# Kernel tuning notes

Hardware: AMD Instinct MI355X
Metric: run time of the kernel (lower is better)

The kernel has to match this reference:

```python
import jax, jax.numpy as jnp
import numpy as np

EMBED, VOCAB, NUM_DIGEST, EXPAND = 128, 50257, 4, 4


def _mueller_hash(k):
    # https://stackoverflow.com/a/12996028 , uint32 wraparound semantics
    k = (k >> np.uint32(16) ^ k) * np.uint32(73244475)
    k = (k >> np.uint32(16) ^ k) * np.uint32(73244475)
    k = k >> np.uint32(16) ^ k
    return k


def setup_inputs() -> dict:
    key = jax.random.key(0)
    k_tok, k_tab, k_w1, k_w2 = jax.random.split(key, 4)
    # bloom ledger hash indices (exact replication of bloom_ledger)
    ids = np.arange(VOCAB, dtype=np.uint32)
    i_list, j_list = [], []
    for _ in range(NUM_DIGEST):
        ids = _mueller_hash(ids)
        i_list.append(ids % VOCAB)
        ids = _mueller_hash(ids)
        j_list.append(ids % VOCAB)
    bloom_i = jnp.asarray(np.concatenate(i_list).astype(np.int32))
    bloom_j = jnp.asarray(np.concatenate(j_list).astype(np.int32))
    hidden = EMBED * EXPAND
    return {
        "tokens": jax.random.randint(k_tok, (8, 4096), 0, VOCAB, dtype=jnp.int32),
        "table": jax.random.normal(k_tab, (VOCAB, EMBED), jnp.float32) / np.sqrt(EMBED),
        "bloom_i": bloom_i,
        "bloom_j": bloom_j,
        "w1": jax.random.normal(k_w1, (EMBED, hidden), jnp.float32) / np.sqrt(EMBED),
        "b1": jnp.zeros((hidden,), jnp.float32),
        "w2": jax.random.normal(k_w2, (hidden, EMBED), jnp.float32) / np.sqrt(hidden),
        "b2": jnp.zeros((EMBED,), jnp.float32),
    }


def reference(tokens, table, bloom_i, bloom_j, w1, b1, w2, b2):
    vocab = table.shape[0]
    num_digest = bloom_i.shape[0] // vocab
    scale = jnp.asarray(1.0 / np.sqrt(num_digest), table.dtype)
    # bloom @ table as a scatter-add: A[i] += scale * table[j]  -> [vocab, embed]
    agg = jnp.zeros_like(table).at[bloom_i].add(scale * table[bloom_j])
    # one_hot(tokens) @ (bloom @ table) == row gather
    x = agg[tokens]                      # [B, S, embed]
    h = jax.nn.gelu(x @ w1 + b1)         # [B, S, hidden]
    return h @ w2 + b2                   # [B, S, embed]
```

## Files before the change

kernel.cpp:

```cpp
#include <hip/hip_runtime.h>
#include <hip/hip_bf16.h>
#include <stdint.h>

#define EMBED  128
#define HIDDEN 512
#define TB     64
#define HHALF  256
#define CAP    32

typedef __attribute__((ext_vector_type(8))) short short8v;
typedef __attribute__((ext_vector_type(4))) float f32x4;

__device__ __forceinline__ ushort f2bf(float f) {
    uint32_t b = __float_as_uint(f);
    uint32_t r = (b + 0x7FFFu + ((b >> 16) & 1u)) >> 16;
    return (ushort)r;
}

__device__ __forceinline__ float gelu_fast(float x) {
    float x2 = x * x;
    float u  = x * fmaf(0.035677408136f, x2, 0.7978845608f);
    float t  = __expf(2.0f * u);
    return x - x * __frcp_rn(t + 1.0f);
}

__global__ __launch_bounds__(256)
void prep_kernel(const float* __restrict__ w1, const float* __restrict__ w2,
                 ushort* __restrict__ W1t, ushort* __restrict__ W2t,
                 int* __restrict__ cnt, int vocab) {
    __shared__ float T[32][33];
    int b = blockIdx.x;
    int t = threadIdx.x;
    if (b < 128) {
        const float* in; ushort* outp; int inCols, outCols, tr, tc;
        if (b < 64) {
            in = w1; outp = W1t; inCols = 512; outCols = 128;
            tr = b >> 4; tc = b & 15;
        } else {
            int b2 = b - 64;
            in = w2; outp = W2t; inCols = 128; outCols = 512;
            tr = b2 >> 2; tc = b2 & 3;
        }
        int r  = t >> 3;
        int c4 = (t & 7) * 4;
        float4 v = *(const float4*)&in[(size_t)(tr * 32 + r) * inCols + tc * 32 + c4];
        T[c4 + 0][r] = v.x; T[c4 + 1][r] = v.y; T[c4 + 2][r] = v.z; T[c4 + 3][r] = v.w;
        __syncthreads();
        ushort o[4];
        #pragma unroll
        for (int i = 0; i < 4; ++i) o[i] = f2bf(T[r][c4 + i]);
        *(ushort4*)&outp[(size_t)(tc * 32 + r) * outCols + tr * 32 + c4] = *(ushort4*)o;
    } else {
        int i = (b - 128) * 256 + t;
        if (i < vocab) cnt[i] = 0;
    }
}

__global__ __launch_bounds__(256)
void bucket_kernel(const int* __restrict__ bi, const int* __restrict__ bj,
                   int* __restrict__ cnt, int* __restrict__ csr, int nk) {
    int k = blockIdx.x * blockDim.x + threadIdx.x;
    if (k >= nk) return;
    int i = bi[k];
    int slot = atomicAdd(&cnt[i], 1);
    if (slot < CAP) csr[(size_t)i * CAP + slot] = bj[k];
}

__global__ __launch_bounds__(512)
void mlp_mfma_kernel(const int*    __restrict__ tokens,
                     const float*  __restrict__ table,
                     const int*    __restrict__ cnt,
                     const int*    __restrict__ csr,
                     const ushort* __restrict__ W1t,
                     const ushort* __restrict__ W2t,
                     const float*  __restrict__ b1,
                     const float*  __restrict__ b2,
                     float*        __restrict__ out) {
    __shared__ ushort Xs[TB * EMBED];
    __shared__ ushort Hs[TB * HHALF];

    const int t    = threadIdx.x;
    const int lane = t & 63;
    const int wv   = t >> 6;
    const int base = blockIdx.x * TB;
    const int l15  = lane & 15;
    const int lhi  = lane >> 4;

    {
        int r    = t >> 3;
        int coff = (t & 7) * 16;
        int tok  = tokens[base + r];
        int m    = min(cnt[tok], CAP);
        const int* jrow = csr + (size_t)tok * CAP;
        f32x4 xa0 = {0.f,0.f,0.f,0.f}, xa1 = {0.f,0.f,0.f,0.f};
        f32x4 xa2 = {0.f,0.f,0.f,0.f}, xa3 = {0.f,0.f,0.f,0.f};
        #pragma unroll 2
        for (int e = 0; e < 8; ++e) {
            int j = (e < m) ? jrow[e] : 0;
            const float* trp = table + (size_t)j * EMBED + coff;
            float4 v0 = *(const float4*)(trp);
            float4 v1 = *(const float4*)(trp + 4);
            float4 v2 = *(const float4*)(trp + 8);
            float4 v3 = *(const float4*)(trp + 12);
            if (e < m) {
                xa0 += (f32x4){v0.x, v0.y, v0.z, v0.w};
                xa1 += (f32x4){v1.x, v1.y, v1.z, v1.w};
                xa2 += (f32x4){v2.x, v2.y, v2.z, v2.w};
                xa3 += (f32x4){v3.x, v3.y, v3.z, v3.w};
            }
        }
        for (int e = 8; e < m; ++e) {
            int j = jrow[e];
            const float* trp = table + (size_t)j * EMBED + coff;
            float4 v0 = *(const float4*)(trp);
            float4 v1 = *(const float4*)(trp + 4);
            float4 v2 = *(const float4*)(trp + 8);
            float4 v3 = *(const float4*)(trp + 12);
            xa0 += (f32x4){v0.x, v0.y, v0.z, v0.w};
            xa1 += (f32x4){v1.x, v1.y, v1.z, v1.w};
            xa2 += (f32x4){v2.x, v2.y, v2.z, v2.w};
            xa3 += (f32x4){v3.x, v3.y, v3.z, v3.w};
        }
        ushort u[16];
        #pragma unroll
        for (int q = 0; q < 4; ++q) {
            u[q]      = f2bf(0.5f * xa0[q]);
            u[4 + q]  = f2bf(0.5f * xa1[q]);
            u[8 + q]  = f2bf(0.5f * xa2[q]);
            u[12 + q] = f2bf(0.5f * xa3[q]);
        }
        int g0 = (t & 7) * 2;
        #pragma unroll
        for (int h = 0; h < 2; ++h)
            *(short8v*)&Xs[r * EMBED + ((g0 + h) ^ (r & 7)) * 8] = *(short8v*)&u[h * 8];
    }
    __syncthreads();

    f32x4 acc2[4];
    {
        float bv = b2[wv * 16 + l15];
        #pragma unroll
        for (int m = 0; m < 4; ++m) acc2[m] = (f32x4){bv, bv, bv, bv};
    }

    #pragma unroll
    for (int h = 0; h < 2; ++h) {
        f32x4 acc1[4][2];
        #pragma unroll
        for (int n = 0; n < 2; ++n) {
            float bv = b1[h * HHALF + wv * 32 + n * 16 + l15];
            #pragma unroll
            for (int m = 0; m < 4; ++m) acc1[m][n] = (f32x4){bv, bv, bv, bv};
        }
        #pragma unroll
        for (int kk = 0; kk < EMBED / 32; ++kk) {
            short8v a[4];
            #pragma unroll
            for (int m = 0; m < 4; ++m) {
                int r = m * 16 + l15;
                int g = (kk * 4 + lhi) ^ (r & 7);
                a[m] = *(const short8v*)&Xs[r * EMBED + g * 8];
            }
            #pragma unroll
            for (int n = 0; n < 2; ++n) {
                int col = h * HHALF + wv * 32 + n * 16 + l15;
                short8v b = *(const short8v*)(W1t + (size_t)col * EMBED + kk * 32 + lhi * 8);
                #pragma unroll
                for (int m = 0; m < 4; ++m)
                    acc1[m][n] = __builtin_amdgcn_mfma_f32_16x16x32_bf16(a[m], b, acc1[m][n], 0, 0, 0);
            }
        }

        #pragma unroll
        for (int n = 0; n < 2; ++n) {
            int colh = wv * 32 + n * 16 + l15;
            #pragma unroll
            for (int m = 0; m < 4; ++m)
                #pragma unroll
                for (int q = 0; q < 4; ++q) {
                    int row = m * 16 + lhi * 4 + q;
                    float hv = gelu_fast(acc1[m][n][q]);
                    int g = (colh >> 3) ^ (row & 7);
                    Hs[row * HHALF + g * 8 + (colh & 7)] = f2bf(hv);
                }
        }
        __syncthreads();

        #pragma unroll
        for (int kk = 0; kk < HHALF / 32; ++kk) {
            short8v a[4];
            #pragma unroll
            for (int m = 0; m < 4; ++m) {
                int r = m * 16 + l15;
                int g = (kk * 4 + lhi) ^ (r & 7);
                a[m] = *(const short8v*)&Hs[r * HHALF + g * 8];
            }
            int col = wv * 16 + l15;
            short8v b = *(const short8v*)(W2t + (size_t)col * HIDDEN + h * HHALF + kk * 32 + lhi * 8);
            #pragma unroll
            for (int m = 0; m < 4; ++m)
                acc2[m] = __builtin_amdgcn_mfma_f32_16x16x32_bf16(a[m], b, acc2[m], 0, 0, 0);
        }
        __syncthreads();
    }

    #pragma unroll
    for (int m = 0; m < 4; ++m)
        #pragma unroll
        for (int q = 0; q < 4; ++q) {
            int row = m * 16 + lhi * 4 + q;
            out[(size_t)(base + row) * EMBED + wv * 16 + l15] = acc2[m][q];
        }
}

extern "C" void kernel_launch(void* const* d_in, const int* in_sizes, int n_in,
                              void* d_out, int out_size, void* d_ws, size_t ws_size,
                              hipStream_t stream) {
    const int*   tokens = (const int*)  d_in[0];
    const float* table  = (const float*)d_in[1];
    const int*   bi     = (const int*)  d_in[2];
    const int*   bj     = (const int*)  d_in[3];
    const float* w1     = (const float*)d_in[4];
    const float* b1     = (const float*)d_in[5];
    const float* w2     = (const float*)d_in[6];
    const float* b2     = (const float*)d_in[7];
    float* out = (float*)d_out;

    const int vocab = in_sizes[1] / EMBED;
    const int nk    = in_sizes[2];
    const int ntok  = in_sizes[0];

    char* ws = (char*)d_ws;
    size_t off = 0;
    auto alloc = [&](size_t b) { size_t o = off; off += (b + 255) & ~(size_t)255; return o; };
    ushort* W1t = (ushort*)(ws + alloc((size_t)EMBED * HIDDEN * 2));
    ushort* W2t = (ushort*)(ws + alloc((size_t)EMBED * HIDDEN * 2));
    int*    csr = (int*)   (ws + alloc((size_t)vocab * CAP * 4));
    int*    cnt = (int*)   (ws + alloc((size_t)vocab * 4));

    int zeroBlocks = (vocab + 255) / 256;
    prep_kernel<<<128 + zeroBlocks, 256, 0, stream>>>(w1, w2, W1t, W2t, cnt, vocab);

    bucket_kernel<<<(nk + 255) / 256, 256, 0, stream>>>(bi, bj, cnt, csr, nk);

    mlp_mfma_kernel<<<ntok / TB, 512, 0, stream>>>(tokens, table, cnt, csr,
                                                   W1t, W2t, b1, b2, out);
}
```

Before: 57.76 us.

## Gather from bf16 table copy, use 16-bit CSR indices, halve token tile

Adds a pass in the prep kernel that converts the whole fp32 embedding table to bf16, so the per-token gather of digest rows reads half the bytes. CSR column indices are stored as ushort, which holds because vocab is below 65536. The MLP tile drops from 64 to 32 tokens per block with a minBlocks launch bound, doubling the grid and lowering LDS use per block for more occupancy. The cost is an extra full-table read and write every call (about 25MB fp32 in, 13MB bf16 out), plus bf16 rounding of table values before summation.

New measurement: 68.89 us. +19.3%, slower.

```diff
diff --git a/kernel.cpp b/kernel.cpp
--- a/kernel.cpp
+++ b/kernel.cpp
@@ -4,7 +4,7 @@
 
 #define EMBED  128
 #define HIDDEN 512
-#define TB     64
+#define TB     32
 #define HHALF  256
 #define CAP    32
 
@@ -15,6 +15,9 @@
     uint32_t b = __float_as_uint(f);
     uint32_t r = (b + 0x7FFFu + ((b >> 16) & 1u)) >> 16;
     return (ushort)r;
+}
+__device__ __forceinline__ float bf2f(ushort u) {
+    return __uint_as_float(((uint32_t)u) << 16);
 }
 
 __device__ __forceinline__ float gelu_fast(float x) {
@@ -27,7 +30,9 @@
 __global__ __launch_bounds__(256)
 void prep_kernel(const float* __restrict__ w1, const float* __restrict__ w2,
                  ushort* __restrict__ W1t, ushort* __restrict__ W2t,
-                 int* __restrict__ cnt, int vocab) {
+                 int* __restrict__ cnt, int vocab,
+                 const float* __restrict__ table, ushort* __restrict__ tbf,
+                 int zb, int n8) {
     __shared__ float T[32][33];
     int b = blockIdx.x;
     int t = threadIdx.x;
@@ -50,27 +55,37 @@
         #pragma unroll
         for (int i = 0; i < 4; ++i) o[i] = f2bf(T[r][c4 + i]);
         *(ushort4*)&outp[(size_t)(tc * 32 + r) * outCols + tr * 32 + c4] = *(ushort4*)o;
-    } else {
+    } else if (b < 128 + zb) {
         int i = (b - 128) * 256 + t;
         if (i < vocab) cnt[i] = 0;
+    } else {
+        int gid = (b - 128 - zb) * 256 + t;
+        if (gid < n8) {
+            const float* src = table + (size_t)gid * 8;
+            float4 v0 = *(const float4*)(src);
+            float4 v1 = *(const float4*)(src + 4);
+            ushort u[8] = {f2bf(v0.x), f2bf(v0.y), f2bf(v0.z), f2bf(v0.w),
+                           f2bf(v1.x), f2bf(v1.y), f2bf(v1.z), f2bf(v1.w)};
+            *(short8v*)&tbf[(size_t)gid * 8] = *(short8v*)u;
+        }
     }
 }
 
 __global__ __launch_bounds__(256)
 void bucket_kernel(const int* __restrict__ bi, const int* __restrict__ bj,
-                   int* __restrict__ cnt, int* __restrict__ csr, int nk) {
+                   int* __restrict__ cnt, ushort* __restrict__ csr, int nk) {
     int k = blockIdx.x * blockDim.x + threadIdx.x;
     if (k >= nk) return;
     int i = bi[k];
     int slot = atomicAdd(&cnt[i], 1);
-    if (slot < CAP) csr[(size_t)i * CAP + slot] = bj[k];
-}
-
-__global__ __launch_bounds__(512)
+    if (slot < CAP) csr[(size_t)i * CAP + slot] = (ushort)bj[k];
+}
+
+__global__ __launch_bounds__(512, 8)
 void mlp_mfma_kernel(const int*    __restrict__ tokens,
-                     const float*  __restrict__ table,
+                     const ushort* __restrict__ tbf,
                      const int*    __restrict__ cnt,
-                     const int*    __restrict__ csr,
+                     const ushort* __restrict__ csr,
                      const ushort* __restrict__ W1t,
                      const ushort* __restrict__ W2t,
                      const float*  __restrict__ b1,
@@ -87,76 +102,55 @@
     const int lhi  = lane >> 4;
 
     {
-        int r    = t >> 3;
-        int coff = (t & 7) * 16;
-        int tok  = tokens[base + r];
-        int m    = min(cnt[tok], CAP);
-        const int* jrow = csr + (size_t)tok * CAP;
-        f32x4 xa0 = {0.f,0.f,0.f,0.f}, xa1 = {0.f,0.f,0.f,0.f};
-        f32x4 xa2 = {0.f,0.f,0.f,0.f}, xa3 = {0.f,0.f,0.f,0.f};
-        #pragma unroll 2
+        int r   = t >> 4;
+        int c8  = t & 15;
+        int tok = tokens[base + r];
+        int m   = min(cnt[tok], CAP);
+        const ushort* jrow = csr + (size_t)tok * CAP;
+        float acc[8] = {0.f,0.f,0.f,0.f,0.f,0.f,0.f,0.f};
+        #pragma unroll
         for (int e = 0; e < 8; ++e) {
-            int j = (e < m) ? jrow[e] : 0;
-            const float* trp = table + (size_t)j * EMBED + coff;
-            float4 v0 = *(const float4*)(trp);
-            float4 v1 = *(const float4*)(trp + 4);
-            float4 v2 = *(const float4*)(trp + 8);
-            float4 v3 = *(const float4*)(trp + 12);
+            int j = (e < m) ? (int)jrow[e] : 0;
+            short8v v = *(const short8v*)&tbf[(size_t)j * EMBED + c8 * 8];
             if (e < m) {
-                xa0 += (f32x4){v0.x, v0.y, v0.z, v0.w};
-                xa1 += (f32x4){v1.x, v1.y, v1.z, v1.w};
-                xa2 += (f32x4){v2.x, v2.y, v2.z, v2.w};
-                xa3 += (f32x4){v3.x, v3.y, v3.z, v3.w};
+                #pragma unroll
+                for (int q = 0; q < 8; ++q) acc[q] += bf2f((ushort)v[q]);
             }
         }
         for (int e = 8; e < m; ++e) {
-            int j = jrow[e];
-            const float* trp = table + (size_t)j * EMBED + coff;
-            float4 v0 = *(const float4*)(trp);
-            float4 v1 = *(const float4*)(trp + 4);
-            float4 v2 = *(const float4*)(trp + 8);
-            float4 v3 = *(const float4*)(trp + 12);
-            xa0 += (f32x4){v0.x, v0.y, v0.z, v0.w};
-            xa1 += (f32x4){v1.x, v1.y, v1.z, v1.w};
-            xa2 += (f32x4){v2.x, v2.y, v2.z, v2.w};
-            xa3 += (f32x4){v3.x, v3.y, v3.z, v3.w};
-        }
-        ushort u[16];
-        #pragma unroll
-        for (int q = 0; q < 4; ++q) {
-            u[q]      = f2bf(0.5f * xa0[q]);
-            u[4 + q]  = f2bf(0.5f * xa1[q]);
-            u[8 + q]  = f2bf(0.5f * xa2[q]);
-            u[12 + q] = f2bf(0.5f * xa3[q]);
-        }
-        int g0 = (t & 7) * 2;
-        #pragma unroll
-        for (int h = 0; h < 2; ++h)
-            *(short8v*)&Xs[r * EMBED + ((g0 + h) ^ (r & 7)) * 8] = *(short8v*)&u[h * 8];
+            int j = (int)jrow[e];
+            short8v v = *(const short8v*)&tbf[(size_t)j * EMBED + c8 * 8];
+            #pragma unroll
+            for (int q = 0; q < 8; ++q) acc[q] += bf2f((ushort)v[q]);
+        }
+        ushort u[8];
+        #pragma unroll
+        for (int q = 0; q < 8; ++q) u[q] = f2bf(0.5f * acc[q]);
+        *(short8v*)&Xs[r * EMBED + (c8 ^ (r & 7)) * 8] = *(short8v*)u;
     }
     __syncthreads();
 
-    f32x4 acc2[4];
+    f32x4 acc2[2];
     {
         float bv = b2[wv * 16 + l15];
-        #pragma unroll
-        for (int m = 0; m < 4; ++m) acc2[m] = (f32x4){bv, bv, bv, bv};
+        acc2[0] = (f32x4){bv, bv, bv, bv};
+        acc2[1] = acc2[0];
     }
 
     #pragma unroll
     for (int h = 0; h < 2; ++h) {
-        f32x4 acc1[4][2];
+        f32x4 acc1[2][2];
         #pragma unroll
         for (int n = 0; n < 2; ++n) {
             float bv = b1[h * HHALF + wv * 32 + n * 16 + l15];
-            #pragma unroll
-            for (int m = 0; m < 4; ++m) acc1[m][n] = (f32x4){bv, bv, bv, bv};
+            acc1[0][n] = (f32x4){bv, bv, bv, bv};
+            acc1[1][n] = acc1[0][n];
         }
         #pragma unroll
         for (int kk = 0; kk < EMBED / 32; ++kk) {
-            short8v a[4];
-            #pragma unroll
-            for (int m = 0; m < 4; ++m) {
+            short8v a[2];
+            #pragma unroll
+            for (int m = 0; m < 2; ++m) {
                 int r = m * 16 + l15;
                 int g = (kk * 4 + lhi) ^ (r & 7);
                 a[m] = *(const short8v*)&Xs[r * EMBED + g * 8];
@@ -166,7 +160,7 @@
                 int col = h * HHALF + wv * 32 + n * 16 + l15;
                 short8v b = *(const short8v*)(W1t + (size_t)col * EMBED + kk * 32 + lhi * 8);
                 #pragma unroll
-                for (int m = 0; m < 4; ++m)
+                for (int m = 0; m < 2; ++m)
                     acc1[m][n] = __builtin_amdgcn_mfma_f32_16x16x32_bf16(a[m], b, acc1[m][n], 0, 0, 0);
             }
         }
@@ -175,7 +169,7 @@
         for (int n = 0; n < 2; ++n) {
             int colh = wv * 32 + n * 16 + l15;
             #pragma unroll
-            for (int m = 0; m < 4; ++m)
+            for (int m = 0; m < 2; ++m)
                 #pragma unroll
                 for (int q = 0; q < 4; ++q) {
                     int row = m * 16 + lhi * 4 + q;
@@ -188,9 +182,9 @@
 
         #pragma unroll
         for (int kk = 0; kk < HHALF / 32; ++kk) {
-            short8v a[4];
-            #pragma unroll
-            for (int m = 0; m < 4; ++m) {
+            short8v a[2];
+            #pragma unroll
+            for (int m = 0; m < 2; ++m) {
                 int r = m * 16 + l15;
                 int g = (kk * 4 + lhi) ^ (r & 7);
                 a[m] = *(const short8v*)&Hs[r * HHALF + g * 8];
@@ -198,14 +192,14 @@
             int col = wv * 16 + l15;
             short8v b = *(const short8v*)(W2t + (size_t)col * HIDDEN + h * HHALF + kk * 32 + lhi * 8);
             #pragma unroll
-            for (int m = 0; m < 4; ++m)
+            for (int m = 0; m < 2; ++m)
                 acc2[m] = __builtin_amdgcn_mfma_f32_16x16x32_bf16(a[m], b, acc2[m], 0, 0, 0);
         }
         __syncthreads();
     }
 
     #pragma unroll
-    for (int m = 0; m < 4; ++m)
+    for (int m = 0; m < 2; ++m)
         #pragma unroll
         for (int q = 0; q < 4; ++q) {
             int row = m * 16 + lhi * 4 + q;
@@ -235,14 +229,18 @@
     auto alloc = [&](size_t b) { size_t o = off; off += (b + 255) & ~(size_t)255; return o; };
     ushort* W1t = (ushort*)(ws + alloc((size_t)EMBED * HIDDEN * 2));
     ushort* W2t = (ushort*)(ws + alloc((size_t)EMBED * HIDDEN * 2));
-    int*    csr = (int*)   (ws + alloc((size_t)vocab * CAP * 4));
+    ushort* tbf = (ushort*)(ws + alloc((size_t)vocab * EMBED * 2));
+    ushort* csr = (ushort*)(ws + alloc((size_t)vocab * CAP * 2));
     int*    cnt = (int*)   (ws + alloc((size_t)vocab * 4));
 
-    int zeroBlocks = (vocab + 255) / 256;
-    prep_kernel<<<128 + zeroBlocks, 256, 0, stream>>>(w1, w2, W1t, W2t, cnt, vocab);
+    int zb = (vocab + 255) / 256;
+    int n8 = vocab * EMBED / 8;
+    int cb = (n8 + 255) / 256;
+    prep_kernel<<<128 + zb + cb, 256, 0, stream>>>(w1, w2, W1t, W2t, cnt, vocab,
+                                                   table, tbf, zb, n8);
 
     bucket_kernel<<<(nk + 255) / 256, 256, 0, stream>>>(bi, bj, cnt, csr, nk);
 
-    mlp_mfma_kernel<<<ntok / TB, 512, 0, stream>>>(tokens, table, cnt, csr,
+    mlp_mfma_kernel<<<ntok / TB, 512, 0, stream>>>(tokens, tbf, cnt, csr,
                                                    W1t, W2t, b1, b2, out);
 }
```
